# Optimization experiments

Measured on AMD Instinct MI355X. Metric: run time of the kernel, lower is better.

Reference implementation:

```python
import jax, jax.numpy as jnp
import numpy as np

S = 9                      # spiral length
V = [8192, 4096, 2048, 1024, 512]  # verts per level, finest -> latent


def grid_sample_bilinear(feat, grid):
    # feat [B,C,H,W], grid [B,P,2] in [-1,1]; bilinear, align_corners=True
    B, C, H, W = feat.shape
    x = (grid[..., 0] + 1.0) * 0.5 * (W - 1)
    y = (grid[..., 1] + 1.0) * 0.5 * (H - 1)
    x0 = jnp.floor(x); y0 = jnp.floor(y)
    wx = x - x0; wy = y - y0
    x0i = jnp.clip(x0.astype(jnp.int32), 0, W - 1)
    x1i = jnp.clip(x0.astype(jnp.int32) + 1, 0, W - 1)
    y0i = jnp.clip(y0.astype(jnp.int32), 0, H - 1)
    y1i = jnp.clip(y0.astype(jnp.int32) + 1, 0, H - 1)
    featf = feat.reshape(B, C, H * W).transpose(0, 2, 1)  # [B,HW,C]
    def gat(yi, xi):
        return jnp.take_along_axis(featf, (yi * W + xi)[..., None], axis=1)  # [B,P,C]
    w00 = ((1 - wy) * (1 - wx))[..., None]
    w01 = ((1 - wy) * wx)[..., None]
    w10 = (wy * (1 - wx))[..., None]
    w11 = (wy * wx)[..., None]
    return gat(y0i, x0i) * w00 + gat(y0i, x1i) * w01 + gat(y1i, x0i) * w10 + gat(y1i, x1i) * w11


def pool(x, row, col, val):
    # sparse mesh upsample: gather cols, scale, scatter-add into rows
    n_out = row.shape[0] // 3
    g = x[:, col, :] * val[None, :, None]                       # [B,nnz,C]
    return jnp.zeros((x.shape[0], n_out, x.shape[-1]), x.dtype).at[:, row, :].add(g)


def dsconv(x, idx, wd, wp, b):
    # depthwise-separable spiral conv: gather spiral ring, depthwise over S, pointwise mix
    g = x[:, idx]                                # [B,N,S,C]
    dw = jnp.einsum('bnsc,sc->bnc', g, wd)       # depthwise over spiral dim
    return jnp.einsum('bnc,co->bno', dw, wp) + b # pointwise


def _forward(uv, feat, upsample, s0, s1, s2, s3,
             row0, col0, val0, row1, col1, val1, row2, col2, val2, row3, col3, val3,
             wd0, wp0, b0, wd1, wp1, b1, wd2, wp2, b2, wd3, wp3, b3, wdh, wph, bh):
    uvc = jnp.clip((uv - 0.5) * 2.0, -1.0, 1.0)
    x = grid_sample_bilinear(feat, uvc)           # [B,P,C]  (torch: [B,C,P] then permute)
    x = jnp.einsum('vp,bpc->bvc', upsample, x)    # [B,V4,C] latent mesh features
    x = jax.nn.relu(dsconv(pool(x, row3, col3, val3), s3, wd0, wp0, b0))  # [B,1024,512]
    x = jax.nn.relu(dsconv(pool(x, row2, col2, val2), s2, wd1, wp1, b1))  # [B,2048,256]
    x = jax.nn.relu(dsconv(pool(x, row1, col1, val1), s1, wd2, wp2, b2))  # [B,4096,128]
    x = jax.nn.relu(dsconv(pool(x, row0, col0, val0), s0, wd3, wp3, b3))  # [B,8192,64]
    return dsconv(x, s0, wdh, wph, bh)            # [B,8192,3]


def setup_inputs():
    ks = jax.random.split(jax.random.key(0), 64)
    B, P, C, H, W = 8, 21, 512, 32, 32
    inp = {}
    inp['uv'] = jax.random.uniform(ks[0], (B, P, 2), jnp.float32)
    inp['feat'] = jax.random.normal(ks[1], (B, C, H, W), jnp.float32)
    inp['upsample'] = 0.01 * jnp.ones((V[4], P), jnp.float32)
    for i in range(4):
        inp[f's{i}'] = jax.random.randint(ks[2 + i], (V[i], S), 0, V[i])
    for i in range(4):
        nnz = 3 * V[i]
        inp[f'row{i}'] = jax.random.randint(ks[6 + 3 * i], (nnz,), 0, V[i])
        inp[f'col{i}'] = jax.random.randint(ks[7 + 3 * i], (nnz,), 0, V[i + 1])
        inp[f'val{i}'] = jax.random.uniform(ks[8 + 3 * i], (nnz,), jnp.float32)
    chans = [(512, 512), (512, 256), (256, 128), (128, 64), (64, 3)]
    names = ['0', '1', '2', '3', 'h']
    k = 20
    for (ci, co), nm in zip(chans, names):
        inp[f'wd{nm}'] = 0.1 * jax.random.normal(ks[k], (S, ci), jnp.float32); k += 1
        inp[f'wp{nm}'] = jax.random.normal(ks[k], (ci, co), jnp.float32) * (1.0 / float(np.sqrt(ci))); k += 1
        inp[f'b{nm}'] = jnp.zeros((co,), jnp.float32); k += 1
    return inp


def reference(uv, feat, upsample, s0, s1, s2, s3,
              row0, col0, val0, row1, col1, val1, row2, col2, val2, row3, col3, val3,
              wd0, wp0, b0, wd1, wp1, b1, wd2, wp2, b2, wd3, wp3, b3, wdh, wph, bh):
    return _forward(uv, feat, upsample, s0, s1, s2, s3,
                    row0, col0, val0, row1, col1, val1, row2, col2, val2, row3, col3, val3,
                    wd0, wp0, b0, wd1, wp1, b1, wd2, wp2, b2, wd3, wp3, b3, wdh, wph, bh)
```

## Files before the change

### kernel.cpp

```cpp
#include <hip/hip_runtime.h>

#define B_  8
#define P_  21
#define H_  32
#define W_  32

typedef float f32x4 __attribute__((ext_vector_type(4)));
typedef _Float16 f16x8 __attribute__((ext_vector_type(8)));

struct CsrParams {
  const int*   row[4];
  const int*   col[4];
  const float* val[4];
  int*   cnt[4];
  int*   rowptr[4];
  int*   colsout[4];
  float* valsout[4];
  int    nnz[4];
  int    V[4];
};

__global__ void count_kernel(CsrParams p) {
  int l = blockIdx.y;
  int k = blockIdx.x * 256 + threadIdx.x;
  if (k < p.nnz[l]) atomicAdd(&p.cnt[l][p.row[l][k]], 1);
}

__global__ void scan_kernel(CsrParams p) {
  int l = blockIdx.x;
  int V = p.V[l];
  int* cnt = p.cnt[l];
  int* rp  = p.rowptr[l];
  int t = threadIdx.x;
  int chunk = V / 256;
  int base = t * chunk;
  int s = 0;
  for (int i = 0; i < chunk; ++i) s += cnt[base + i];
  __shared__ int sm[256];
  sm[t] = s;
  __syncthreads();
  for (int off = 1; off < 256; off <<= 1) {
    int v = (t >= off) ? sm[t - off] : 0;
    __syncthreads();
    sm[t] += v;
    __syncthreads();
  }
  int run = sm[t] - s;
  for (int i = 0; i < chunk; ++i) {
    int c = cnt[base + i];
    rp[base + i]  = run;
    cnt[base + i] = run;
    run += c;
  }
  if (t == 255) rp[V] = run;
}

__global__ void fill_kernel(CsrParams p) {
  int l = blockIdx.y;
  int k = blockIdx.x * 256 + threadIdx.x;
  if (k < p.nnz[l]) {
    int r = p.row[l][k];
    int pos = atomicAdd(&p.cnt[l][r], 1);
    p.colsout[l][pos] = p.col[l][k];
    p.valsout[l][pos] = p.val[l][k];
  }
}

__global__ void sample_kernel(const float* __restrict__ uv,
                              const float* __restrict__ feat,
                              float* __restrict__ xs) {
  int bp = blockIdx.x;
  int b  = bp / P_;
  float u0 = uv[bp * 2 + 0], u1 = uv[bp * 2 + 1];
  float gx = fminf(fmaxf((u0 - 0.5f) * 2.0f, -1.0f), 1.0f);
  float gy = fminf(fmaxf((u1 - 0.5f) * 2.0f, -1.0f), 1.0f);
  float fx = (gx + 1.0f) * 0.5f * (W_ - 1);
  float fy = (gy + 1.0f) * 0.5f * (H_ - 1);
  float x0f = floorf(fx), y0f = floorf(fy);
  float wx = fx - x0f, wy = fy - y0f;
  int x0 = (int)x0f, y0 = (int)y0f;
  int x0i = min(max(x0, 0), W_ - 1), x1i = min(max(x0 + 1, 0), W_ - 1);
  int y0i = min(max(y0, 0), H_ - 1), y1i = min(max(y0 + 1, 0), H_ - 1);
  float w00 = (1.f - wy) * (1.f - wx), w01 = (1.f - wy) * wx;
  float w10 = wy * (1.f - wx),        w11 = wy * wx;
  for (int c = threadIdx.x; c < 512; c += blockDim.x) {
    const float* fb = feat + ((size_t)(b * 512 + c)) * (H_ * W_);
    float v = fb[y0i * W_ + x0i] * w00 + fb[y0i * W_ + x1i] * w01 +
              fb[y1i * W_ + x0i] * w10 + fb[y1i * W_ + x1i] * w11;
    xs[(size_t)bp * 512 + c] = v;
  }
}

__global__ void upsample_kernel(const float* __restrict__ up,
                                const float* __restrict__ xs,
                                float* __restrict__ xu) {
  int v = blockIdx.x, b = blockIdx.y;
  int c4 = threadIdx.x << 2;
  float4 acc = make_float4(0.f, 0.f, 0.f, 0.f);
  for (int p = 0; p < P_; ++p) {
    float u = up[v * P_ + p];
    const float4 xv = *(const float4*)&xs[((size_t)(b * P_ + p)) * 512 + c4];
    acc.x = fmaf(u, xv.x, acc.x);
    acc.y = fmaf(u, xv.y, acc.y);
    acc.z = fmaf(u, xv.z, acc.z);
    acc.w = fmaf(u, xv.w, acc.w);
  }
  *(float4*)&xu[((size_t)(b * 512 + v)) * 512 + c4] = acc;
}

__global__ __launch_bounds__(256) void pool_kernel(
    const float* __restrict__ x,
    const int* __restrict__ rowptr,
    const int* __restrict__ cols,
    const float* __restrict__ vals,
    float* __restrict__ out,
    int Vout, int Vin, int Cin) {
  const int lpr    = Cin >> 3;
  const int lshift = 31 - __clz(lpr);
  const int rpb    = 256 >> lshift;
  const int lr = threadIdx.x >> lshift;
  const int lc = threadIdx.x & (lpr - 1);
  const int b  = blockIdx.x & 7;
  const int n  = (blockIdx.x >> 3) * rpb + lr;
  const int c8 = lc << 3;
  const float* xb = x + (size_t)b * Vin * Cin + c8;
  int j0 = rowptr[n], j1 = rowptr[n + 1];
  float4 a0 = make_float4(0.f, 0.f, 0.f, 0.f);
  float4 a1 = make_float4(0.f, 0.f, 0.f, 0.f);
  for (int j = j0; j < j1; ++j) {
    float v = vals[j];
    const float* xr = xb + (size_t)cols[j] * Cin;
    float4 x0 = *(const float4*)xr;
    float4 x1 = *(const float4*)(xr + 4);
    a0.x = fmaf(v, x0.x, a0.x); a0.y = fmaf(v, x0.y, a0.y);
    a0.z = fmaf(v, x0.z, a0.z); a0.w = fmaf(v, x0.w, a0.w);
    a1.x = fmaf(v, x1.x, a1.x); a1.y = fmaf(v, x1.y, a1.y);
    a1.z = fmaf(v, x1.z, a1.z); a1.w = fmaf(v, x1.w, a1.w);
  }
  float* op = &out[((size_t)b * Vout + n) * Cin + c8];
  *(float4*)op = a0;
  *(float4*)(op + 4) = a1;
}

__global__ __launch_bounds__(256) void dw_split_kernel(
    const float* __restrict__ xin,
    const int* __restrict__ sidx,
    const float* __restrict__ wd,
    _Float16* __restrict__ a0o,
    _Float16* __restrict__ a1o,
    int Vout, int Cin) {
  const int lpr    = Cin >> 3;
  const int lshift = 31 - __clz(lpr);
  const int rpb    = 256 >> lshift;
  const int lr = threadIdx.x >> lshift;
  const int lc = threadIdx.x & (lpr - 1);
  const int b  = blockIdx.x & 7;
  const int n  = (blockIdx.x >> 3) * rpb + lr;
  const int c8 = lc << 3;
  const float* xb = xin + (size_t)b * Vout * Cin + c8;

  int idx[9];
  #pragma unroll
  for (int s = 0; s < 9; ++s) idx[s] = sidx[n * 9 + s];

  float4 a0 = make_float4(0.f, 0.f, 0.f, 0.f);
  float4 a1 = make_float4(0.f, 0.f, 0.f, 0.f);
  #pragma unroll
  for (int s = 0; s < 9; ++s) {
    const float* xr = xb + (size_t)idx[s] * Cin;
    float4 x0 = *(const float4*)xr;
    float4 x1 = *(const float4*)(xr + 4);
    const float* wr = wd + s * Cin + c8;
    float4 w0 = *(const float4*)wr;
    float4 w1 = *(const float4*)(wr + 4);
    a0.x = fmaf(w0.x, x0.x, a0.x); a0.y = fmaf(w0.y, x0.y, a0.y);
    a0.z = fmaf(w0.z, x0.z, a0.z); a0.w = fmaf(w0.w, x0.w, a0.w);
    a1.x = fmaf(w1.x, x1.x, a1.x); a1.y = fmaf(w1.y, x1.y, a1.y);
    a1.z = fmaf(w1.z, x1.z, a1.z); a1.w = fmaf(w1.w, x1.w, a1.w);
  }

  size_t m = (size_t)b * Vout + n;
  float v[8] = {a0.x, a0.y, a0.z, a0.w, a1.x, a1.y, a1.z, a1.w};
  f16x8 hi, lo;
  #pragma unroll
  for (int i = 0; i < 8; ++i) {
    _Float16 h0 = (_Float16)v[i];
    float r = (v[i] - (float)h0) * 2048.0f;
    hi[i] = h0;
    lo[i] = (_Float16)r;
  }
  *(f16x8*)&a0o[m * Cin + c8] = hi;
  *(f16x8*)&a1o[m * Cin + c8] = lo;
}

__global__ void bsplit_kernel(const float* __restrict__ wp,
                              _Float16* __restrict__ b0,
                              _Float16* __restrict__ b1,
                              int K, int N) {
  int idx = blockIdx.x * 256 + threadIdx.x;
  if (idx >= N * K) return;
  int n = idx / K, k = idx - n * K;
  float v = wp[(size_t)k * N + n];
  _Float16 h0 = (_Float16)v;
  float r = (v - (float)h0) * 2048.0f;
  b0[idx] = h0;
  b1[idx] = (_Float16)r;
}

__global__ __launch_bounds__(256) void gemm_f16x2(
    const _Float16* __restrict__ A0, const _Float16* __restrict__ A1,
    const _Float16* __restrict__ Bt0, const _Float16* __restrict__ Bt1,
    const float* __restrict__ bias, float* __restrict__ C,
    int M, int N, int K) {
  constexpr int RP = 72;
  __shared__ _Float16 As[2][128][RP];
  __shared__ _Float16 Bs[2][64][RP];
  const int tid = threadIdx.x;
  const int bx = blockIdx.x;
  const int xr_ = (bx & 7) * (gridDim.x >> 3) + (bx >> 3);
  const int m0 = xr_ * 128, n0 = blockIdx.y * 64;
  const int wid = tid >> 6, lane = tid & 63;
  const int wr = wid >> 1, wc = wid & 1;
  const int lo = lane & 15, hi = lane >> 4;

  f32x4 accM[4][2], accC[4][2];
  #pragma unroll
  for (int mi = 0; mi < 4; ++mi)
    #pragma unroll
    for (int nj = 0; nj < 2; ++nj) {
      accM[mi][nj] = (f32x4){0.f, 0.f, 0.f, 0.f};
      accC[mi][nj] = (f32x4){0.f, 0.f, 0.f, 0.f};
    }

  const _Float16* gA[2] = {A0, A1};
  const _Float16* gB[2] = {Bt0, Bt1};

  for (int k0 = 0; k0 < K; k0 += 64) {
    #pragma unroll
    for (int p = 0; p < 2; ++p) {
      #pragma unroll
      for (int i = 0; i < 4; ++i) {
        int c = tid + 256 * i;
        int r = c >> 3, k8 = (c & 7) << 3;
        uint4 v = *(const uint4*)(gA[p] + (size_t)(m0 + r) * K + k0 + k8);
        *(uint4*)&As[p][r][k8] = v;
      }
      #pragma unroll
      for (int i = 0; i < 2; ++i) {
        int c = tid + 256 * i;
        int r = c >> 3, k8 = (c & 7) << 3;
        uint4 v = *(const uint4*)(gB[p] + (size_t)(n0 + r) * K + k0 + k8);
        *(uint4*)&Bs[p][r][k8] = v;
      }
    }
    __syncthreads();
    #pragma unroll
    for (int s = 0; s < 2; ++s) {
      const int kk = s * 32 + hi * 8;
      f16x8 af[4][2], bf[2][2];
      #pragma unroll
      for (int mi = 0; mi < 4; ++mi) {
        af[mi][0] = *(const f16x8*)&As[0][wr * 64 + mi * 16 + lo][kk];
        af[mi][1] = *(const f16x8*)&As[1][wr * 64 + mi * 16 + lo][kk];
      }
      #pragma unroll
      for (int nj = 0; nj < 2; ++nj) {
        bf[nj][0] = *(const f16x8*)&Bs[0][wc * 32 + nj * 16 + lo][kk];
        bf[nj][1] = *(const f16x8*)&Bs[1][wc * 32 + nj * 16 + lo][kk];
      }
      #pragma unroll
      for (int mi = 0; mi < 4; ++mi)
        #pragma unroll
        for (int nj = 0; nj < 2; ++nj) {
          accM[mi][nj] = __builtin_amdgcn_mfma_f32_16x16x32_f16(
              af[mi][0], bf[nj][0], accM[mi][nj], 0, 0, 0);
          accC[mi][nj] = __builtin_amdgcn_mfma_f32_16x16x32_f16(
              af[mi][0], bf[nj][1], accC[mi][nj], 0, 0, 0);
          accC[mi][nj] = __builtin_amdgcn_mfma_f32_16x16x32_f16(
              af[mi][1], bf[nj][0], accC[mi][nj], 0, 0, 0);
        }
    }
    __syncthreads();
  }

  const float INV = 1.0f / 2048.0f;
  #pragma unroll
  for (int mi = 0; mi < 4; ++mi)
    #pragma unroll
    for (int nj = 0; nj < 2; ++nj) {
      int col = n0 + wc * 32 + nj * 16 + lo;
      float bv = bias[col];
      #pragma unroll
      for (int r = 0; r < 4; ++r) {
        int row = m0 + wr * 64 + mi * 16 + hi * 4 + r;
        float v = accM[mi][nj][r] + accC[mi][nj][r] * INV + bv;
        v = fmaxf(v, 0.f);
        C[(size_t)row * N + col] = v;
      }
    }
}

__global__ __launch_bounds__(256) void dw_kernel(const float* __restrict__ xin,
                          const int* __restrict__ sidx,
                          const float* __restrict__ wd,
                          float* __restrict__ out,
                          int Vout, int Cin) {
  const int lpr    = Cin >> 3;
  const int lshift = 31 - __clz(lpr);
  const int rpb    = 256 >> lshift;
  const int lr = threadIdx.x >> lshift;
  const int lc = threadIdx.x & (lpr - 1);
  const int b  = blockIdx.x & 7;
  const int n  = (blockIdx.x >> 3) * rpb + lr;
  const int c8 = lc << 3;
  const float* xb = xin + (size_t)b * Vout * Cin + c8;

  int idx[9];
  #pragma unroll
  for (int s = 0; s < 9; ++s) idx[s] = sidx[n * 9 + s];

  float4 a0 = make_float4(0.f, 0.f, 0.f, 0.f);
  float4 a1 = make_float4(0.f, 0.f, 0.f, 0.f);
  #pragma unroll
  for (int s = 0; s < 9; ++s) {
    const float* xr = xb + (size_t)idx[s] * Cin;
    float4 x0 = *(const float4*)xr;
    float4 x1 = *(const float4*)(xr + 4);
    const float* wr = wd + s * Cin + c8;
    float4 w0 = *(const float4*)wr;
    float4 w1 = *(const float4*)(wr + 4);
    a0.x = fmaf(w0.x, x0.x, a0.x); a0.y = fmaf(w0.y, x0.y, a0.y);
    a0.z = fmaf(w0.z, x0.z, a0.z); a0.w = fmaf(w0.w, x0.w, a0.w);
    a1.x = fmaf(w1.x, x1.x, a1.x); a1.y = fmaf(w1.y, x1.y, a1.y);
    a1.z = fmaf(w1.z, x1.z, a1.z); a1.w = fmaf(w1.w, x1.w, a1.w);
  }
  float* op = &out[((size_t)b * Vout + n) * Cin + c8];
  *(float4*)op = a0;
  *(float4*)(op + 4) = a1;
}

__global__ void head_kernel(const float* __restrict__ dw,
                            const float* __restrict__ wph,
                            const float* __restrict__ bh,
                            float* __restrict__ out) {
  int bx = blockIdx.x;
  int bid = (bx & 7) * (gridDim.x >> 3) + (bx >> 3);
  int lane = threadIdx.x & 63;
  int rowLocal = threadIdx.x >> 6;
  int row = bid * 4 + rowLocal;
  float d = dw[(size_t)row * 64 + lane];
  float a0 = d * wph[lane * 3 + 0];
  float a1 = d * wph[lane * 3 + 1];
  float a2 = d * wph[lane * 3 + 2];
  for (int off = 32; off > 0; off >>= 1) {
    a0 += __shfl_down(a0, off);
    a1 += __shfl_down(a1, off);
    a2 += __shfl_down(a2, off);
  }
  if (lane == 0) {
    out[(size_t)row * 3 + 0] = a0 + bh[0];
    out[(size_t)row * 3 + 1] = a1 + bh[1];
    out[(size_t)row * 3 + 2] = a2 + bh[2];
  }
}

extern "C" void kernel_launch(void* const* d_in, const int* in_sizes, int n_in,
                              void* d_out, int out_size, void* d_ws, size_t ws_size,
                              hipStream_t stream) {
  const float* uv   = (const float*)d_in[0];
  const float* feat = (const float*)d_in[1];
  const float* up   = (const float*)d_in[2];
  const int* sArr[4] = {(const int*)d_in[3], (const int*)d_in[4],
                        (const int*)d_in[5], (const int*)d_in[6]};

  const size_t SLAB = 8ull * 2048 * 512;
  float* Wf = (float*)d_ws;
  float* S0 = Wf;
  float* S1 = Wf + SLAB;
  _Float16* A0 = (_Float16*)(S1 + SLAB);
  _Float16* A1 = A0 + SLAB;
  _Float16* Bt0 = (_Float16*)(S0 + 4500000);
  _Float16* Bt1 = Bt0 + 262144;
  float* xs = (float*)(A1 + SLAB);
  int* ib = (int*)(xs + (size_t)B_ * P_ * 512);
  float* HD = (float*)A0;

  int Vt[4] = {1024, 2048, 4096, 8192};
  int NZ[4] = {3072, 6144, 12288, 24576};
  int* cnt[4]; int* rp[4]; int* co[4]; float* va[4];
  {
    int* pc = ib;
    for (int t = 0; t < 4; ++t) { cnt[t] = pc; pc += Vt[t]; }
    for (int t = 0; t < 4; ++t) { rp[t] = pc; pc += Vt[t] + 1; }
    for (int t = 0; t < 4; ++t) { co[t] = pc; pc += NZ[t]; }
    float* pv = (float*)pc;
    for (int t = 0; t < 4; ++t) { va[t] = pv; pv += NZ[t]; }
  }

  CsrParams cp;
  for (int t = 0; t < 4; ++t) {
    int i = 3 - t;
    cp.row[t] = (const int*)d_in[7 + 3 * i];
    cp.col[t] = (const int*)d_in[8 + 3 * i];
    cp.val[t] = (const float*)d_in[9 + 3 * i];
    cp.cnt[t] = cnt[t]; cp.rowptr[t] = rp[t];
    cp.colsout[t] = co[t]; cp.valsout[t] = va[t];
    cp.nnz[t] = NZ[t]; cp.V[t] = Vt[t];
  }

  sample_kernel<<<B_ * P_, 256, 0, stream>>>(uv, feat, xs);
  upsample_kernel<<<dim3(512, B_), 128, 0, stream>>>(up, xs, S0);

  hipMemsetAsync(ib, 0, 15360 * sizeof(int), stream);
  count_kernel<<<dim3(96, 4), 256, 0, stream>>>(cp);
  scan_kernel<<<4, 256, 0, stream>>>(cp);
  fill_kernel<<<dim3(96, 4), 256, 0, stream>>>(cp);

  struct Stg { int Vin, Vout, Cin, Cout; const int* s; const float *wd, *wp, *bias; };
  Stg st[4] = {
    {512, 1024, 512, 512, sArr[3], (const float*)d_in[19], (const float*)d_in[20], (const float*)d_in[21]},
    {1024, 2048, 512, 256, sArr[2], (const float*)d_in[22], (const float*)d_in[23], (const float*)d_in[24]},
    {2048, 4096, 256, 128, sArr[1], (const float*)d_in[25], (const float*)d_in[26], (const float*)d_in[27]},
    {4096, 8192, 128, 64, sArr[0], (const float*)d_in[28], (const float*)d_in[29], (const float*)d_in[30]},
  };

  for (int t = 0; t < 4; ++t) {
    int rpb = 2048 / st[t].Cin;
    pool_kernel<<<8 * (st[t].Vout / rpb), 256, 0, stream>>>(
        S0, rp[t], co[t], va[t], S1, st[t].Vout, st[t].Vin, st[t].Cin);
    dw_split_kernel<<<8 * (st[t].Vout / rpb), 256, 0, stream>>>(
        S1, st[t].s, st[t].wd, A0, A1, st[t].Vout, st[t].Cin);
    int KK = st[t].Cin, NN = st[t].Cout;
    bsplit_kernel<<<(KK * NN + 255) / 256, 256, 0, stream>>>(
        st[t].wp, Bt0, Bt1, KK, NN);
    int M = B_ * st[t].Vout;
    gemm_f16x2<<<dim3(M / 128, NN / 64), 256, 0, stream>>>(
        A0, A1, Bt0, Bt1, st[t].bias, S0, M, NN, KK);
  }

  dw_kernel<<<8 * (8192 / 32), 256, 0, stream>>>(
      S0, sArr[0], (const float*)d_in[31], HD, 8192, 64);
  head_kernel<<<(B_ * 8192) / 4, 256, 0, stream>>>(
      HD, (const float*)d_in[32], (const float*)d_in[33], (float*)d_out);
}
```

Measured before the change: 289.5 us.

## Fuse CSR build, batch weight splits, and fuse head depthwise with projection

Replaces the memset plus count, scan and fill kernels with one kernel per level that counts and scans in shared memory. It also merges the four per-stage weight-split launches into one launch that writes into separate offsets. The head depthwise conv and the 3-channel projection are fused so the intermediate buffer is never written or re-read. Together these cut launch count and global traffic. The cost is a CSR build that runs on only 4 blocks.

```diff
diff --git a/kernel.cpp b/kernel.cpp
--- a/kernel.cpp
+++ b/kernel.cpp
@@ -12,7 +12,6 @@
   const int*   row[4];
   const int*   col[4];
   const float* val[4];
-  int*   cnt[4];
   int*   rowptr[4];
   int*   colsout[4];
   float* valsout[4];
@@ -20,49 +19,52 @@
   int    V[4];
 };
 
-__global__ void count_kernel(CsrParams p) {
-  int l = blockIdx.y;
-  int k = blockIdx.x * 256 + threadIdx.x;
-  if (k < p.nnz[l]) atomicAdd(&p.cnt[l][p.row[l][k]], 1);
-}
-
-__global__ void scan_kernel(CsrParams p) {
-  int l = blockIdx.x;
-  int V = p.V[l];
-  int* cnt = p.cnt[l];
-  int* rp  = p.rowptr[l];
-  int t = threadIdx.x;
-  int chunk = V / 256;
-  int base = t * chunk;
+__global__ __launch_bounds__(1024) void csr_build_kernel(CsrParams p) {
+  __shared__ int cnt[8192];
+  __shared__ int partial[1024];
+  const int l   = blockIdx.x;
+  const int V   = p.V[l];
+  const int nnz = p.nnz[l];
+  const int t   = threadIdx.x;
+  const int* row = p.row[l];
+
+  for (int i = t; i < V; i += 1024) cnt[i] = 0;
+  __syncthreads();
+  for (int k = t; k < nnz; k += 1024) atomicAdd(&cnt[row[k]], 1);
+  __syncthreads();
+
+  const int chunk = V >> 10;
+  const int base  = t * chunk;
   int s = 0;
   for (int i = 0; i < chunk; ++i) s += cnt[base + i];
-  __shared__ int sm[256];
-  sm[t] = s;
+  partial[t] = s;
   __syncthreads();
-  for (int off = 1; off < 256; off <<= 1) {
-    int v = (t >= off) ? sm[t - off] : 0;
+  for (int off = 1; off < 1024; off <<= 1) {
+    int v = (t >= off) ? partial[t - off] : 0;
     __syncthreads();
-    sm[t] += v;
+    partial[t] += v;
     __syncthreads();
   }
-  int run = sm[t] - s;
+  int run = partial[t] - s;
+  int* rp = p.rowptr[l];
   for (int i = 0; i < chunk; ++i) {
     int c = cnt[base + i];
     rp[base + i]  = run;
     cnt[base + i] = run;
     run += c;
   }
-  if (t == 255) rp[V] = run;
-}
-
-__global__ void fill_kernel(CsrParams p) {
-  int l = blockIdx.y;
-  int k = blockIdx.x * 256 + threadIdx.x;
-  if (k < p.nnz[l]) {
-    int r = p.row[l][k];
-    int pos = atomicAdd(&p.cnt[l][r], 1);
-    p.colsout[l][pos] = p.col[l][k];
-    p.valsout[l][pos] = p.val[l][k];
+  if (t == 1023) rp[V] = nnz;
+  __syncthreads();
+
+  const int*   col = p.col[l];
+  const float* val = p.val[l];
+  int*   co = p.colsout[l];
+  float* va = p.valsout[l];
+  for (int k = t; k < nnz; k += 1024) {
+    int r = row[k];
+    int pos = atomicAdd(&cnt[r], 1);
+    co[pos] = col[k];
+    va[pos] = val[k];
   }
 }
 
@@ -193,18 +195,29 @@
   *(f16x8*)&a1o[m * Cin + c8] = lo;
 }
 
-__global__ void bsplit_kernel(const float* __restrict__ wp,
-                              _Float16* __restrict__ b0,
-                              _Float16* __restrict__ b1,
-                              int K, int N) {
+struct BsplitParams {
+  const float* wp[4];
+  int K[4], N[4], off[4];
+  _Float16* b0;
+  _Float16* b1;
+};
+
+__global__ void bsplit_all_kernel(BsplitParams p) {
   int idx = blockIdx.x * 256 + threadIdx.x;
-  if (idx >= N * K) return;
-  int n = idx / K, k = idx - n * K;
-  float v = wp[(size_t)k * N + n];
-  _Float16 h0 = (_Float16)v;
-  float r = (v - (float)h0) * 2048.0f;
-  b0[idx] = h0;
-  b1[idx] = (_Float16)r;
+  #pragma unroll
+  for (int t = 0; t < 4; ++t) {
+    int sz = p.N[t] * p.K[t];
+    if (idx < sz) {
+      int n = idx / p.K[t], k = idx - n * p.K[t];
+      float v = p.wp[t][(size_t)k * p.N[t] + n];
+      _Float16 h0 = (_Float16)v;
+      float r = (v - (float)h0) * 2048.0f;
+      p.b0[p.off[t] + idx] = h0;
+      p.b1[p.off[t] + idx] = (_Float16)r;
+      return;
+    }
+    idx -= sz;
+  }
 }
 
 __global__ __launch_bounds__(256) void gemm_f16x2(
@@ -300,67 +313,42 @@
     }
 }
 
-__global__ __launch_bounds__(256) void dw_kernel(const float* __restrict__ xin,
-                          const int* __restrict__ sidx,
-                          const float* __restrict__ wd,
-                          float* __restrict__ out,
-                          int Vout, int Cin) {
-  const int lpr    = Cin >> 3;
-  const int lshift = 31 - __clz(lpr);
-  const int rpb    = 256 >> lshift;
-  const int lr = threadIdx.x >> lshift;
-  const int lc = threadIdx.x & (lpr - 1);
-  const int b  = blockIdx.x & 7;
-  const int n  = (blockIdx.x >> 3) * rpb + lr;
-  const int c8 = lc << 3;
-  const float* xb = xin + (size_t)b * Vout * Cin + c8;
+__global__ __launch_bounds__(256) void head_fused_kernel(
+    const float* __restrict__ x,
+    const int* __restrict__ sidx,
+    const float* __restrict__ wdh,
+    const float* __restrict__ wph,
+    const float* __restrict__ bh,
+    float* __restrict__ out) {
+  const int bid  = blockIdx.x;
+  const int b    = bid & 7;
+  const int wid  = threadIdx.x >> 6;
+  const int lane = threadIdx.x & 63;
+  const int n    = (bid >> 3) * 4 + wid;
+  const float* xb = x + (size_t)b * 8192 * 64 + lane;
 
   int idx[9];
   #pragma unroll
   for (int s = 0; s < 9; ++s) idx[s] = sidx[n * 9 + s];
 
-  float4 a0 = make_float4(0.f, 0.f, 0.f, 0.f);
-  float4 a1 = make_float4(0.f, 0.f, 0.f, 0.f);
-  #pragma unroll
-  for (int s = 0; s < 9; ++s) {
-    const float* xr = xb + (size_t)idx[s] * Cin;
-    float4 x0 = *(const float4*)xr;
-    float4 x1 = *(const float4*)(xr + 4);
-    const float* wr = wd + s * Cin + c8;
-    float4 w0 = *(const float4*)wr;
-    float4 w1 = *(const float4*)(wr + 4);
-    a0.x = fmaf(w0.x, x0.x, a0.x); a0.y = fmaf(w0.y, x0.y, a0.y);
-    a0.z = fmaf(w0.z, x0.z, a0.z); a0.w = fmaf(w0.w, x0.w, a0.w);
-    a1.x = fmaf(w1.x, x1.x, a1.x); a1.y = fmaf(w1.y, x1.y, a1.y);
-    a1.z = fmaf(w1.z, x1.z, a1.z); a1.w = fmaf(w1.w, x1.w, a1.w);
-  }
-  float* op = &out[((size_t)b * Vout + n) * Cin + c8];
-  *(float4*)op = a0;
-  *(float4*)(op + 4) = a1;
-}
-
-__global__ void head_kernel(const float* __restrict__ dw,
-                            const float* __restrict__ wph,
-                            const float* __restrict__ bh,
-                            float* __restrict__ out) {
-  int bx = blockIdx.x;
-  int bid = (bx & 7) * (gridDim.x >> 3) + (bx >> 3);
-  int lane = threadIdx.x & 63;
-  int rowLocal = threadIdx.x >> 6;
-  int row = bid * 4 + rowLocal;
-  float d = dw[(size_t)row * 64 + lane];
-  float a0 = d * wph[lane * 3 + 0];
-  float a1 = d * wph[lane * 3 + 1];
-  float a2 = d * wph[lane * 3 + 2];
+  float acc = 0.f;
+  #pragma unroll
+  for (int s = 0; s < 9; ++s)
+    acc = fmaf(wdh[s * 64 + lane], xb[(size_t)idx[s] * 64], acc);
+
+  float a0 = acc * wph[lane * 3 + 0];
+  float a1 = acc * wph[lane * 3 + 1];
+  float a2 = acc * wph[lane * 3 + 2];
   for (int off = 32; off > 0; off >>= 1) {
     a0 += __shfl_down(a0, off);
     a1 += __shfl_down(a1, off);
     a2 += __shfl_down(a2, off);
   }
   if (lane == 0) {
-    out[(size_t)row * 3 + 0] = a0 + bh[0];
-    out[(size_t)row * 3 + 1] = a1 + bh[1];
-    out[(size_t)row * 3 + 2] = a2 + bh[2];
+    size_t row = (size_t)b * 8192 + n;
+    out[row * 3 + 0] = a0 + bh[0];
+    out[row * 3 + 1] = a1 + bh[1];
+    out[row * 3 + 2] = a2 + bh[2];
   }
 }
 
@@ -379,18 +367,16 @@
   float* S1 = Wf + SLAB;
   _Float16* A0 = (_Float16*)(S1 + SLAB);
   _Float16* A1 = A0 + SLAB;
-  _Float16* Bt0 = (_Float16*)(S0 + 4500000);
-  _Float16* Bt1 = Bt0 + 262144;
+  _Float16* Bt0all = (_Float16*)(S0 + 4500000);
+  _Float16* Bt1all = Bt0all + 434176;
   float* xs = (float*)(A1 + SLAB);
   int* ib = (int*)(xs + (size_t)B_ * P_ * 512);
-  float* HD = (float*)A0;
 
   int Vt[4] = {1024, 2048, 4096, 8192};
   int NZ[4] = {3072, 6144, 12288, 24576};
-  int* cnt[4]; int* rp[4]; int* co[4]; float* va[4];
+  int* rp[4]; int* co[4]; float* va[4];
   {
     int* pc = ib;
-    for (int t = 0; t < 4; ++t) { cnt[t] = pc; pc += Vt[t]; }
     for (int t = 0; t < 4; ++t) { rp[t] = pc; pc += Vt[t] + 1; }
     for (int t = 0; t < 4; ++t) { co[t] = pc; pc += NZ[t]; }
     float* pv = (float*)pc;
@@ -403,18 +389,14 @@
     cp.row[t] = (const int*)d_in[7 + 3 * i];
     cp.col[t] = (const int*)d_in[8 + 3 * i];
     cp.val[t] = (const float*)d_in[9 + 3 * i];
-    cp.cnt[t] = cnt[t]; cp.rowptr[t] = rp[t];
+    cp.rowptr[t] = rp[t];
     cp.colsout[t] = co[t]; cp.valsout[t] = va[t];
     cp.nnz[t] = NZ[t]; cp.V[t] = Vt[t];
   }
 
+  csr_build_kernel<<<4, 1024, 0, stream>>>(cp);
   sample_kernel<<<B_ * P_, 256, 0, stream>>>(uv, feat, xs);
   upsample_kernel<<<dim3(512, B_), 128, 0, stream>>>(up, xs, S0);
-
-  hipMemsetAsync(ib, 0, 15360 * sizeof(int), stream);
-  count_kernel<<<dim3(96, 4), 256, 0, stream>>>(cp);
-  scan_kernel<<<4, 256, 0, stream>>>(cp);
-  fill_kernel<<<dim3(96, 4), 256, 0, stream>>>(cp);
 
   struct Stg { int Vin, Vout, Cin, Cout; const int* s; const float *wd, *wp, *bias; };
   Stg st[4] = {
@@ -424,22 +406,30 @@
     {4096, 8192, 128, 64, sArr[0], (const float*)d_in[28], (const float*)d_in[29], (const float*)d_in[30]},
   };
 
+  BsplitParams bp;
+  int boff = 0;
+  for (int t = 0; t < 4; ++t) {
+    bp.wp[t] = st[t].wp;
+    bp.K[t] = st[t].Cin; bp.N[t] = st[t].Cout;
+    bp.off[t] = boff;
+    boff += st[t].Cin * st[t].Cout;
+  }
+  bp.b0 = Bt0all; bp.b1 = Bt1all;
+  bsplit_all_kernel<<<(boff + 255) / 256, 256, 0, stream>>>(bp);
+
   for (int t = 0; t < 4; ++t) {
     int rpb = 2048 / st[t].Cin;
     pool_kernel<<<8 * (st[t].Vout / rpb), 256, 0, stream>>>(
         S0, rp[t], co[t], va[t], S1, st[t].Vout, st[t].Vin, st[t].Cin);
     dw_split_kernel<<<8 * (st[t].Vout / rpb), 256, 0, stream>>>(
         S1, st[t].s, st[t].wd, A0, A1, st[t].Vout, st[t].Cin);
-    int KK = st[t].Cin, NN = st[t].Cout;
-    bsplit_kernel<<<(KK * NN + 255) / 256, 256, 0, stream>>>(
-        st[t].wp, Bt0, Bt1, KK, NN);
     int M = B_ * st[t].Vout;
-    gemm_f16x2<<<dim3(M / 128, NN / 64), 256, 0, stream>>>(
-        A0, A1, Bt0, Bt1, st[t].bias, S0, M, NN, KK);
-  }
-
-  dw_kernel<<<8 * (8192 / 32), 256, 0, stream>>>(
-      S0, sArr[0], (const float*)d_in[31], HD, 8192, 64);
-  head_kernel<<<(B_ * 8192) / 4, 256, 0, stream>>>(
-      HD, (const float*)d_in[32], (const float*)d_in[33], (float*)d_out);
-}
+    gemm_f16x2<<<dim3(M / 128, st[t].Cout / 64), 256, 0, stream>>>(
+        A0, A1, Bt0all + bp.off[t], Bt1all + bp.off[t],
+        st[t].bias, S0, M, st[t].Cout, st[t].Cin);
+  }
+
+  head_fused_kernel<<<8 * (8192 / 4), 256, 0, stream>>>(
+      S0, sArr[0], (const float*)d_in[31], (const float*)d_in[32],
+      (const float*)d_in[33], (float*)d_out);
+}
```

Result: slower. 298.9 us (+3.3%).
